# Optimization experiments

Measured on AMD Instinct MI355X. Metric: run time of the kernel, lower is better.

## Reference

```python
import jax, jax.numpy as jnp
import numpy as np

N_HEADS = 16

def setup_inputs() -> dict:
    key = jax.random.key(0)
    k1, k2, k3 = jax.random.split(key, 3)
    B, T, C = 4, 2048, 1024
    x = jax.random.normal(k1, (B, T, C), dtype=jnp.float32)
    w_qkv = jax.random.normal(k2, (C, 3 * C), dtype=jnp.float32) * (1.0 / np.sqrt(C))
    w_out = jax.random.normal(k3, (C, C), dtype=jnp.float32) * (1.0 / np.sqrt(C))
    return {"x": x, "w_qkv": w_qkv, "w_out": w_out}

def reference(x, w_qkv, w_out):
    B, T, C = x.shape
    H = N_HEADS
    D = C // H
    qkv = jnp.einsum('btc,cf->btf', x, w_qkv).reshape(B, T, 3, H, D)
    q, k, v = qkv[:, :, 0], qkv[:, :, 1], qkv[:, :, 2]  # [B,T,H,D]
    q = q.transpose(0, 2, 1, 3)  # [B,H,T,D]
    k = k.transpose(0, 2, 1, 3)
    v = v.transpose(0, 2, 1, 3)
    scale = 1.0 / jnp.sqrt(jnp.asarray(D, dtype=x.dtype))
    scores = jnp.einsum('bhqd,bhkd->bhqk', q, k) * scale  # [B,H,T,T]
    causal = jnp.tril(jnp.ones((T, T), dtype=bool))
    scores = jnp.where(causal[None, None], scores, jnp.asarray(-jnp.inf, dtype=scores.dtype))
    attn = jax.nn.softmax(scores, axis=-1)
    ctx = jnp.einsum('bhqk,bhkd->bhqd', attn, v)  # [B,H,T,D]
    ctx = ctx.transpose(0, 2, 1, 3).reshape(B, T, C)
    return jnp.einsum('btc,co->bto', ctx, w_out)
```

## Files before the change

### kernel.cpp

```cpp
#include <hip/hip_runtime.h>

typedef __attribute__((ext_vector_type(8))) short bf16x8;
typedef __attribute__((ext_vector_type(4))) short bf16x4;
typedef __attribute__((ext_vector_type(4))) float f32x4;
typedef __attribute__((ext_vector_type(4))) unsigned short u16x4;

#define MFMA16(a, b, c) __builtin_amdgcn_mfma_f32_16x16x32_bf16((a), (b), (c), 0, 0, 0)
#define MFMA16K16(a, b, c) __builtin_amdgcn_mfma_f32_16x16x16bf16_1k((a), (b), (c), 0, 0, 0)

__device__ __forceinline__ unsigned short f2bf(float f) {
    union { float f; unsigned int u; } x; x.f = f;
    unsigned int r = x.u + 0x7FFFu + ((x.u >> 16) & 1u);
    return (unsigned short)(r >> 16);
}
__device__ __forceinline__ void gload_lds16(const void* g, void* l) {
    __builtin_amdgcn_global_load_lds(
        (const __attribute__((address_space(1))) unsigned int*)g,
        (__attribute__((address_space(3))) unsigned int*)l,
        16, 0, 0);
}

__global__ void cast_x(const float* __restrict__ in, unsigned short* __restrict__ hi,
                       int n) {
    int i = (blockIdx.x * blockDim.x + threadIdx.x) * 4;
    if (i >= n) return;
    float4 v = *(const float4*)(in + i);
    float vv[4] = {v.x, v.y, v.z, v.w};
    u16x4 h;
#pragma unroll
    for (int j = 0; j < 4; ++j) h[j] = f2bf(vv[j]);
    *(u16x4*)(hi + i) = h;
}

__global__ void tcast_k(const float* __restrict__ in, unsigned short* __restrict__ out,
                        int K, int N) {
    __shared__ float tile[64][65];
    int n0 = blockIdx.x * 64, k0 = blockIdx.y * 64;
    for (int i = threadIdx.x; i < 4096; i += 256) {
        int r = i >> 6, c = i & 63;
        tile[r][c] = in[(size_t)(k0 + r) * N + n0 + c];
    }
    __syncthreads();
    for (int i = threadIdx.x; i < 4096; i += 256) {
        int r = i >> 6, c = i & 63;
        out[(size_t)(n0 + r) * K + k0 + c] = f2bf(tile[c][r]);
    }
}

__global__ __launch_bounds__(256, 2) void gemm_qkv(
    const unsigned short* __restrict__ A,
    const unsigned short* __restrict__ Bt,
    unsigned short* __restrict__ qout, unsigned short* __restrict__ kout,
    unsigned short* __restrict__ vtout, int* __restrict__ counter) {
    const int K = 1024;
    __shared__ __align__(16) unsigned short smem[17408];
    unsigned short* sA = smem;
    unsigned short* sB = smem + 8192;
    int tid = threadIdx.x, lane = tid & 63, w = tid >> 6;
    int c = lane & 15, quad = lane >> 4;
    int sw = c & 7;
    int wm = (w >> 1) * 64, wn = (w & 1) * 64;

    if (tid == 0) *counter = 1024;

    int wg = blockIdx.y * 24 + blockIdx.x;
    int nid = (wg & 7) * 192 + (wg >> 3);
    int m_blk = nid / 24, n_blk = nid - m_blk * 24;
    int m0 = m_blk * 128, n0 = n_blk * 128;

    f32x4 acc[4][4];
#pragma unroll
    for (int i = 0; i < 4; i++)
#pragma unroll
        for (int j = 0; j < 4; j++) acc[i][j] = (f32x4){0.f, 0.f, 0.f, 0.f};

    for (int kk = 0; kk < K; kk += 64) {
#pragma unroll
        for (int p = 0; p < 4; ++p) {
            int ch = p * 256 + tid;
            int r = ch >> 3;
            int gs = (ch & 7) ^ (r & 7);
            gload_lds16(A + (size_t)(m0 + r) * K + kk + gs * 8, &sA[ch * 8]);
            gload_lds16(Bt + (size_t)(n0 + r) * K + kk + gs * 8, &sB[ch * 8]);
        }
        __syncthreads();
#pragma unroll
        for (int ks8 = 0; ks8 < 8; ks8 += 4) {
            bf16x8 af[4], bfr[4];
#pragma unroll
            for (int mt = 0; mt < 4; ++mt)
                af[mt] = *(const bf16x8*)&sA[(wm + mt * 16 + c) * 64 +
                                             ((ks8 + quad) ^ sw) * 8];
#pragma unroll
            for (int nt = 0; nt < 4; ++nt)
                bfr[nt] = *(const bf16x8*)&sB[(wn + nt * 16 + c) * 64 +
                                              ((ks8 + quad) ^ sw) * 8];
#pragma unroll
            for (int mt = 0; mt < 4; ++mt)
#pragma unroll
                for (int nt = 0; nt < 4; ++nt)
                    acc[mt][nt] = MFMA16(af[mt], bfr[nt], acc[mt][nt]);
        }
        __syncthreads();
    }

    const float QSCALE = 0.1803368801111601f;
    bool vreg = (n0 >= 2048);
    if (!vreg) {
        float scale = (n0 < 1024) ? QSCALE : 1.0f;
#pragma unroll
        for (int mt = 0; mt < 4; ++mt)
#pragma unroll
            for (int nt = 0; nt < 4; ++nt)
#pragma unroll
                for (int r = 0; r < 4; ++r)
                    smem[(wm + mt * 16 + quad * 4 + r) * 136 + wn + nt * 16 + c] =
                        f2bf(acc[mt][nt][r] * scale);
    } else {
#pragma unroll
        for (int mt = 0; mt < 4; ++mt)
#pragma unroll
            for (int nt = 0; nt < 4; ++nt)
#pragma unroll
                for (int r = 0; r < 4; ++r)
                    smem[(wn + nt * 16 + c) * 136 + wm + mt * 16 + quad * 4 + r] =
                        f2bf(acc[mt][nt][r]);
    }
    __syncthreads();

    int rr = tid >> 4, cc = tid & 15;
    if (!vreg) {
        int col = n0 + cc * 8;
        int which = col >> 10;
        int h = (col >> 6) & 15, d = col & 63;
        unsigned short* dst = which ? kout : qout;
#pragma unroll
        for (int j = 0; j < 8; ++j) {
            int row = rr + j * 16;
            int grow = m0 + row;
            int b = grow >> 11, t = grow & 2047;
            size_t bh_ = (size_t)(b * 16 + h);
            bf16x8 vv = *(const bf16x8*)&smem[row * 136 + cc * 8];
            *(bf16x8*)&dst[(bh_ * 2048 + t) * 64 + d] = vv;
        }
    } else {
        int grow = m0 + cc * 8;
        int b = grow >> 11, t = grow & 2047;
#pragma unroll
        for (int j = 0; j < 8; ++j) {
            int nrow = rr + j * 16;
            int col = n0 + nrow;
            int h = (col >> 6) & 15, d = col & 63;
            size_t bh_ = (size_t)(b * 16 + h);
            bf16x8 vv = *(const bf16x8*)&smem[nrow * 136 + cc * 8];
            *(bf16x8*)&vtout[(bh_ * 64 + d) * 2048 + t] = vv;
        }
    }
}

__global__ __launch_bounds__(256, 2) void gemm2_bt(
    const unsigned short* __restrict__ A,
    const unsigned short* __restrict__ Bt,
    float* __restrict__ out) {
    const int K = 1024, N = 1024;
    __shared__ __align__(16) unsigned short sA[128 * 64], sB[128 * 64];
    int tid = threadIdx.x, lane = tid & 63, w = tid >> 6;
    int c = lane & 15, quad = lane >> 4;
    int sw = c & 7;
    int wm = (w >> 1) * 64, wn = (w & 1) * 64;

    int wg = blockIdx.y * 8 + blockIdx.x;
    int nid = (wg & 7) * 64 + (wg >> 3);
    int m_blk = nid >> 3, n_blk = nid & 7;
    int m0 = m_blk * 128, n0 = n_blk * 128;

    f32x4 acc[4][4];
#pragma unroll
    for (int i = 0; i < 4; i++)
#pragma unroll
        for (int j = 0; j < 4; j++) acc[i][j] = (f32x4){0.f, 0.f, 0.f, 0.f};

    for (int kk = 0; kk < K; kk += 64) {
#pragma unroll
        for (int p = 0; p < 4; ++p) {
            int ch = p * 256 + tid;
            int r = ch >> 3;
            int gs = (ch & 7) ^ (r & 7);
            gload_lds16(A + (size_t)(m0 + r) * K + kk + gs * 8, &sA[ch * 8]);
            gload_lds16(Bt + (size_t)(n0 + r) * K + kk + gs * 8, &sB[ch * 8]);
        }
        __syncthreads();
#pragma unroll
        for (int ks8 = 0; ks8 < 8; ks8 += 4) {
            bf16x8 af[4], bfr[4];
#pragma unroll
            for (int mt = 0; mt < 4; ++mt)
                af[mt] = *(const bf16x8*)&sA[(wm + mt * 16 + c) * 64 +
                                             ((ks8 + quad) ^ sw) * 8];
#pragma unroll
            for (int nt = 0; nt < 4; ++nt)
                bfr[nt] = *(const bf16x8*)&sB[(wn + nt * 16 + c) * 64 +
                                              ((ks8 + quad) ^ sw) * 8];
#pragma unroll
            for (int mt = 0; mt < 4; ++mt)
#pragma unroll
                for (int nt = 0; nt < 4; ++nt)
                    acc[mt][nt] = MFMA16(af[mt], bfr[nt], acc[mt][nt]);
        }
        __syncthreads();
    }

#pragma unroll
    for (int mt = 0; mt < 4; ++mt)
#pragma unroll
        for (int nt = 0; nt < 4; ++nt)
#pragma unroll
            for (int r = 0; r < 4; ++r) {
                int row = m0 + wm + mt * 16 + quad * 4 + r;
                int col = n0 + wn + nt * 16 + c;
                out[(size_t)row * N + col] = acc[mt][nt][r];
            }
}

#define SSTR 72
__device__ const int JOB_ORDER[24] = {7, 15, 23, 14, 22, 6,  13, 21, 12, 20, 5,  11,
                                      19, 10, 18, 4,  9,  17, 8,  16, 3,  2,  1,  0};

__global__ __launch_bounds__(256, 4) void attn_k(
    const unsigned short* __restrict__ q,
    const unsigned short* __restrict__ k,
    const unsigned short* __restrict__ vt,
    unsigned short* __restrict__ ctx,
    float* __restrict__ op, float* __restrict__ lbuf,
    int* __restrict__ counter) {
    const int T = 2048, D = 64;
    __shared__ __align__(16) unsigned short sK[2][64 * SSTR];
    __shared__ __align__(16) unsigned short sV[2][64 * SSTR];
    __shared__ int sNext;

    int tid = threadIdx.x, lane = tid & 63, w = tid >> 6;
    int c = lane & 15, quad = lane >> 4;
    int dv = tid >> 3, tcv = (tid & 7) * 8;

    int qi = blockIdx.x;
    while (qi < 1536) {
        int rank = qi >> 6, bh = qi & 63;
        int t = JOB_ORDER[rank];
        int jt, kt0, nkt;
        bool split, has_diag;
        if (t < 8)       { jt = t;     kt0 = 0;      nkt = 2 * t + 2; split = false; has_diag = true; }
        else if (t < 16) { jt = t;     kt0 = 0;      nkt = jt + 1;    split = true;  has_diag = false; }
        else             { jt = t - 8; kt0 = jt + 1; nkt = jt + 1;    split = true;  has_diag = true; }
        int kt_end = kt0 + nkt;
        int b = bh >> 4, hh = bh & 15;

        const unsigned short* qh = q + (size_t)bh * T * D;
        const unsigned short* kh = k + (size_t)bh * T * D;
        const unsigned short* vh = vt + (size_t)bh * D * T;

        int q0 = jt * 128;
        int qloc = w * 16 + c;
        int qrow[2];
        qrow[0] = q0 + qloc;
        qrow[1] = qrow[0] + 64;

        bf16x8 bq[2][2];
#pragma unroll
        for (int g = 0; g < 2; ++g) {
            bq[g][0] = *(const bf16x8*)&qh[(size_t)qrow[g] * D + quad * 8];
            bq[g][1] = *(const bf16x8*)&qh[(size_t)qrow[g] * D + 32 + quad * 8];
        }

        f32x4 o[2][4];
#pragma unroll
        for (int g = 0; g < 2; ++g)
#pragma unroll
            for (int nt = 0; nt < 4; ++nt) o[g][nt] = (f32x4){0.f, 0.f, 0.f, 0.f};
        float l_i[2] = {0.f, 0.f};

        int kb0 = kt0 * 64;
        bf16x8 kr0 = *(const bf16x8*)&kh[(size_t)(kb0 + lane) * D + w * 8];
        bf16x8 kr1 = *(const bf16x8*)&kh[(size_t)(kb0 + lane) * D + w * 8 + 32];
        bf16x8 vr0 = *(const bf16x8*)&vh[(size_t)dv * T + kb0 + tcv];
        bf16x8 vr1 = *(const bf16x8*)&vh[(size_t)(dv + 32) * T + kb0 + tcv];
        *(bf16x8*)&sK[0][lane * SSTR + w * 8] = kr0;
        *(bf16x8*)&sK[0][lane * SSTR + w * 8 + 32] = kr1;
        *(bf16x8*)&sV[0][dv * SSTR + tcv] = vr0;
        *(bf16x8*)&sV[0][(dv + 32) * SSTR + tcv] = vr1;
        __syncthreads();

        int cur = 0;
        for (int kt = kt0; kt < kt_end; ++kt) {
            int kb = kt * 64;
            if (kt + 1 < kt_end) {
                int kb2 = kb + 64;
                kr0 = *(const bf16x8*)&kh[(size_t)(kb2 + lane) * D + w * 8];
                kr1 = *(const bf16x8*)&kh[(size_t)(kb2 + lane) * D + w * 8 + 32];
                vr0 = *(const bf16x8*)&vh[(size_t)dv * T + kb2 + tcv];
                vr1 = *(const bf16x8*)&vh[(size_t)(dv + 32) * T + kb2 + tcv];
            }
            bool g0_active = !has_diag || (kt != 2 * jt + 1);

            const unsigned short* sKc = sK[cur];
            const unsigned short* sVc = sV[cur];

            f32x4 st[2][4];
            __builtin_amdgcn_s_setprio(1);
#pragma unroll
            for (int mt = 0; mt < 4; ++mt) {
                bf16x8 ak0 = *(const bf16x8*)&sKc[(mt * 16 + c) * SSTR + quad * 8];
                bf16x8 ak1 = *(const bf16x8*)&sKc[(mt * 16 + c) * SSTR + 32 + quad * 8];
#pragma unroll
                for (int g = 0; g < 2; ++g) {
                    f32x4 z = (f32x4){0.f, 0.f, 0.f, 0.f};
                    z = MFMA16(ak0, bq[g][0], z);
                    z = MFMA16(ak1, bq[g][1], z);
                    st[g][mt] = z;
                }
            }
            __builtin_amdgcn_s_setprio(0);

            bf16x4 pf[2][4];
#pragma unroll
            for (int g = 0; g < 2; ++g) {
                if (g == 0 && !g0_active) continue;
                bool diag = has_diag && (kb == q0 + (g << 6));
                if (diag) {
#pragma unroll
                    for (int mt = 0; mt < 4; ++mt)
#pragma unroll
                        for (int r = 0; r < 4; ++r)
                            if (mt * 16 + quad * 4 + r > qloc) st[g][mt][r] = -1.0e30f;
                }
                float rs = 0.f;
#pragma unroll
                for (int mt = 0; mt < 4; ++mt) {
                    float p0 = __builtin_exp2f(st[g][mt][0]);
                    float p1 = __builtin_exp2f(st[g][mt][1]);
                    float p2 = __builtin_exp2f(st[g][mt][2]);
                    float p3 = __builtin_exp2f(st[g][mt][3]);
                    rs += (p0 + p1) + (p2 + p3);
                    unsigned int w0, w1;
                    asm("v_cvt_pk_bf16_f32 %0, %1, %2" : "=v"(w0) : "v"(p0), "v"(p1));
                    asm("v_cvt_pk_bf16_f32 %0, %1, %2" : "=v"(w1) : "v"(p2), "v"(p3));
                    uint2 pk; pk.x = w0; pk.y = w1;
                    pf[g][mt] = *(bf16x4*)&pk;
                }
                l_i[g] += rs;
            }

            __builtin_amdgcn_s_setprio(1);
#pragma unroll
            for (int mt = 0; mt < 4; ++mt) {
#pragma unroll
                for (int nt = 0; nt < 4; ++nt) {
                    bf16x4 av = *(const bf16x4*)&sVc[(nt * 16 + c) * SSTR + mt * 16 + quad * 4];
                    if (g0_active) o[0][nt] = MFMA16K16(av, pf[0][mt], o[0][nt]);
                    o[1][nt] = MFMA16K16(av, pf[1][mt], o[1][nt]);
                }
            }
            __builtin_amdgcn_s_setprio(0);

            if (kt + 1 < kt_end) {
                int nxt = cur ^ 1;
                *(bf16x8*)&sK[nxt][lane * SSTR + w * 8] = kr0;
                *(bf16x8*)&sK[nxt][lane * SSTR + w * 8 + 32] = kr1;
                *(bf16x8*)&sV[nxt][dv * SSTR + tcv] = vr0;
                *(bf16x8*)&sV[nxt][(dv + 32) * SSTR + tcv] = vr1;
                __syncthreads();
                cur = nxt;
            }
        }

        if (tid == 0) sNext = atomicAdd(counter, 1);

        if (!split) {
#pragma unroll
            for (int g = 0; g < 2; ++g) {
                float l = l_i[g];
                l += __shfl_xor(l, 16);
                l += __shfl_xor(l, 32);
                float inv = 1.0f / l;
#pragma unroll
                for (int nt = 0; nt < 4; ++nt) {
                    u16x4 ob;
#pragma unroll
                    for (int r = 0; r < 4; ++r) ob[r] = f2bf(o[g][nt][r] * inv);
                    *(u16x4*)&ctx[(size_t)(b * T + qrow[g]) * 1024 + hh * 64 + nt * 16 + quad * 4] = ob;
                }
            }
        } else {
            int piece = has_diag ? 1 : 0;
            int sidx = bh * 8 + (jt - 8);
            size_t base = (size_t)(piece * 512 + sidx) * 128;
#pragma unroll
            for (int g = 0; g < 2; ++g) {
                float l = l_i[g];
                l += __shfl_xor(l, 16);
                l += __shfl_xor(l, 32);
                int rloc = qrow[g] - q0;
                if (quad == 0) lbuf[base + rloc] = l;
                float* orow = op + (base + rloc) * 64;
#pragma unroll
                for (int nt = 0; nt < 4; ++nt)
                    *(f32x4*)&orow[nt * 16 + quad * 4] = o[g][nt];
            }
        }

        __syncthreads();
        qi = sNext;
    }
}

__global__ void merge_k(const float* __restrict__ op, const float* __restrict__ lbuf,
                        unsigned short* __restrict__ ctx) {
    int gid = blockIdx.x * 256 + threadIdx.x;
    int row = gid >> 4, dq = (gid & 15) * 4;
    int sidx = row >> 7, rloc = row & 127;
    int bh = sidx >> 3, jt = 8 + (sidx & 7);
    int b = bh >> 4, hh = bh & 15;
    int tq = jt * 128 + rloc;
    float inv = 1.0f / (lbuf[row] + lbuf[65536 + row]);
    float4 o0 = *(const float4*)(op + (size_t)row * 64 + dq);
    float4 o1 = *(const float4*)(op + (size_t)(65536 + row) * 64 + dq);
    u16x4 ob;
    ob[0] = f2bf((o0.x + o1.x) * inv);
    ob[1] = f2bf((o0.y + o1.y) * inv);
    ob[2] = f2bf((o0.z + o1.z) * inv);
    ob[3] = f2bf((o0.w + o1.w) * inv);
    *(u16x4*)&ctx[((size_t)(b * 2048 + tq)) * 1024 + hh * 64 + dq] = ob;
}

extern "C" void kernel_launch(void* const* d_in, const int* in_sizes, int n_in,
                              void* d_out, int out_size, void* d_ws, size_t ws_size,
                              hipStream_t stream) {
    const float* x     = (const float*)d_in[0];
    const float* w_qkv = (const float*)d_in[1];
    const float* w_out = (const float*)d_in[2];
    float* out = (float*)d_out;

    char* ws = (char*)d_ws;
    unsigned short* wqkvt = (unsigned short*)(ws + 0);
    unsigned short* woutt = (unsigned short*)(ws + 6291456);
    unsigned short* x_bf  = (unsigned short*)(ws + 8388608);
    unsigned short* qb    = (unsigned short*)(ws + 25165824);
    unsigned short* kb    = (unsigned short*)(ws + 41943040);
    unsigned short* vtb   = (unsigned short*)(ws + 58720256);
    unsigned short* ctx   = (unsigned short*)(ws + 8388608);

    float* op    = (float*)d_out;
    float* lbuf  = (float*)ws;
    int* counter = (int*)(ws + 524288);

    cast_x<<<8192, 256, 0, stream>>>(x, x_bf, 8388608);
    tcast_k<<<dim3(48, 16), 256, 0, stream>>>(w_qkv, wqkvt, 1024, 3072);
    tcast_k<<<dim3(16, 16), 256, 0, stream>>>(w_out, woutt, 1024, 1024);
    gemm_qkv<<<dim3(24, 64), 256, 0, stream>>>(x_bf, wqkvt, qb, kb, vtb, counter);
    attn_k<<<1024, 256, 0, stream>>>(qb, kb, vtb, ctx, op, lbuf, counter);
    merge_k<<<4096, 256, 0, stream>>>(op, lbuf, ctx);
    gemm2_bt<<<dim3(8, 64), 256, 0, stream>>>(ctx, woutt, out);
}
```

Before: 252.1 us.

## Use per-XCD work queues in attention so heads stay local to one L2

Replaces the single global atomic work counter with eight per-XCD counters. Each workgroup reads its XCD id and pulls jobs for a fixed subset of eight batch-heads, stealing from other XCDs' queues once its own runs dry, so K/V for a head tend to be reused within one XCD's L2. It also precomputes K/V prefetch pointers and advances them each iteration instead of recomputing addresses, and resets the counters with a memset rather than inside the QKV GEMM. The risks are an extra memset launch, more atomics, and a possibly less balanced longest-first ordering within each queue.

```diff
diff --git a/kernel.cpp b/kernel.cpp
--- a/kernel.cpp
+++ b/kernel.cpp
@@ -51,7 +51,7 @@
     const unsigned short* __restrict__ A,
     const unsigned short* __restrict__ Bt,
     unsigned short* __restrict__ qout, unsigned short* __restrict__ kout,
-    unsigned short* __restrict__ vtout, int* __restrict__ counter) {
+    unsigned short* __restrict__ vtout) {
     const int K = 1024;
     __shared__ __align__(16) unsigned short smem[17408];
     unsigned short* sA = smem;
@@ -60,8 +60,6 @@
     int c = lane & 15, quad = lane >> 4;
     int sw = c & 7;
     int wm = (w >> 1) * 64, wn = (w & 1) * 64;
-
-    if (tid == 0) *counter = 1024;
 
     int wg = blockIdx.y * 24 + blockIdx.x;
     int nid = (wg & 7) * 192 + (wg >> 3);
@@ -232,7 +230,7 @@
     const unsigned short* __restrict__ vt,
     unsigned short* __restrict__ ctx,
     float* __restrict__ op, float* __restrict__ lbuf,
-    int* __restrict__ counter) {
+    int* __restrict__ counters) {
     const int T = 2048, D = 64;
     __shared__ __align__(16) unsigned short sK[2][64 * SSTR];
     __shared__ __align__(16) unsigned short sV[2][64 * SSTR];
@@ -242,9 +240,24 @@
     int c = lane & 15, quad = lane >> 4;
     int dv = tid >> 3, tcv = (tid & 7) * 8;
 
-    int qi = blockIdx.x;
-    while (qi < 1536) {
-        int rank = qi >> 6, bh = qi & 63;
+    unsigned int xcd;
+    asm volatile("s_getreg_b32 %0, hwreg(HW_REG_XCC_ID)" : "=s"(xcd));
+    int grp = xcd & 7;
+
+    int tries = 0;
+    while (tries < 8) {
+        if (tid == 0) sNext = atomicAdd(&counters[grp << 5], 1);
+        __syncthreads();
+        int qi = sNext;
+        if (qi >= 192) {
+            grp = (grp + 1) & 7;
+            ++tries;
+            __syncthreads();
+            continue;
+        }
+        tries = 0;
+
+        int rank = qi >> 3, bh = grp * 8 + (qi & 7);
         int t = JOB_ORDER[rank];
         int jt, kt0, nkt;
         bool split, has_diag;
@@ -289,15 +302,21 @@
         *(bf16x8*)&sV[0][(dv + 32) * SSTR + tcv] = vr1;
         __syncthreads();
 
+        const unsigned short* kpre = kh + (size_t)(kb0 + 64 + lane) * D + w * 8;
+        const unsigned short* vpre0 = vh + (size_t)dv * T + kb0 + 64 + tcv;
+        const unsigned short* vpre1 = vh + (size_t)(dv + 32) * T + kb0 + 64 + tcv;
+
         int cur = 0;
         for (int kt = kt0; kt < kt_end; ++kt) {
             int kb = kt * 64;
             if (kt + 1 < kt_end) {
-                int kb2 = kb + 64;
-                kr0 = *(const bf16x8*)&kh[(size_t)(kb2 + lane) * D + w * 8];
-                kr1 = *(const bf16x8*)&kh[(size_t)(kb2 + lane) * D + w * 8 + 32];
-                vr0 = *(const bf16x8*)&vh[(size_t)dv * T + kb2 + tcv];
-                vr1 = *(const bf16x8*)&vh[(size_t)(dv + 32) * T + kb2 + tcv];
+                kr0 = *(const bf16x8*)kpre;
+                kr1 = *(const bf16x8*)(kpre + 32);
+                vr0 = *(const bf16x8*)vpre0;
+                vr1 = *(const bf16x8*)vpre1;
+                kpre += 64 * D;
+                vpre0 += 64;
+                vpre1 += 64;
             }
             bool g0_active = !has_diag || (kt != 2 * jt + 1);
 
@@ -372,8 +391,6 @@
             }
         }
 
-        if (tid == 0) sNext = atomicAdd(counter, 1);
-
         if (!split) {
 #pragma unroll
             for (int g = 0; g < 2; ++g) {
@@ -408,7 +425,6 @@
         }
 
         __syncthreads();
-        qi = sNext;
     }
 }
 
@@ -448,15 +464,16 @@
     unsigned short* vtb   = (unsigned short*)(ws + 58720256);
     unsigned short* ctx   = (unsigned short*)(ws + 8388608);
 
-    float* op    = (float*)d_out;
-    float* lbuf  = (float*)ws;
-    int* counter = (int*)(ws + 524288);
+    float* op     = (float*)d_out;
+    float* lbuf   = (float*)ws;
+    int* counters = (int*)(ws + 524288);
 
     cast_x<<<8192, 256, 0, stream>>>(x, x_bf, 8388608);
     tcast_k<<<dim3(48, 16), 256, 0, stream>>>(w_qkv, wqkvt, 1024, 3072);
     tcast_k<<<dim3(16, 16), 256, 0, stream>>>(w_out, woutt, 1024, 1024);
-    gemm_qkv<<<dim3(24, 64), 256, 0, stream>>>(x_bf, wqkvt, qb, kb, vtb, counter);
-    attn_k<<<1024, 256, 0, stream>>>(qb, kb, vtb, ctx, op, lbuf, counter);
+    gemm_qkv<<<dim3(24, 64), 256, 0, stream>>>(x_bf, wqkvt, qb, kb, vtb);
+    hipMemsetAsync(counters, 0, 1024, stream);
+    attn_k<<<1024, 256, 0, stream>>>(qb, kb, vtb, ctx, op, lbuf, counters);
     merge_k<<<4096, 256, 0, stream>>>(op, lbuf, ctx);
     gemm2_bt<<<dim3(8, 64), 256, 0, stream>>>(ctx, woutt, out);
 }
```

Result: slower. 270.7 us (+7.3%).
